# Kernel optimization log

Measured on AMD Instinct MI355X. Metric: run time of the kernel, lower is better.

The kernel has to match this reference:

```python
import jax, jax.numpy as jnp
import numpy as np

NUM_E = 50000
EMBED_DIM = 128
HID_DIM = 200
B = 512
N = 50  # candidate_num / history length
ITER_NUM = 3
ALPHA = 0.5
WEIGHT_BASE = 1.0
SQUASH_W = 1.0
SQUASH_EPS = 1e-9
L2_EPS = 1e-12  # torch F.normalize default eps


def setup_inputs() -> dict:
    key = jax.random.key(0)
    k1, k2, k3, k4, k5, k6, k7 = jax.random.split(key, 7)
    idx = jax.random.randint(k1, (B, N), 0, NUM_E)
    times = jax.random.randint(k2, (B, N), 0, 365)
    # embeddings: normal then row-wise L2 normalize (as in init_embeddings)
    emb = jax.random.normal(k3, (NUM_E, EMBED_DIM), dtype=jnp.float32)
    embeddings = emb / jnp.maximum(jnp.linalg.norm(emb, axis=1, keepdims=True), L2_EPS)
    Ws_w = jax.random.normal(k4, (HID_DIM, EMBED_DIM), dtype=jnp.float32) * (2.0 / (HID_DIM + EMBED_DIM)) ** 0.5
    Ws_b = jnp.zeros((HID_DIM,), dtype=jnp.float32)
    mlp_w = jax.random.normal(k5, (NUM_E, HID_DIM), dtype=jnp.float32) * (2.0 / (NUM_E + HID_DIM)) ** 0.5
    mlp_b = jnp.zeros((NUM_E,), dtype=jnp.float32)
    return {"idx": idx, "times": times, "embeddings": embeddings,
            "Ws_w": Ws_w, "Ws_b": Ws_b, "mlp_w": mlp_w, "mlp_b": mlp_b}


def _squash(s):
    # s: [B, H]; squash over last axis (original axis=-2 on [B,1,1,H,1])
    sq = jnp.sum(s * s, axis=-1, keepdims=True)
    scale = sq / (SQUASH_W + sq) / jnp.sqrt(sq + SQUASH_EPS)
    return scale * s


def reference(idx, times, embeddings, Ws_w, Ws_b, mlp_w, mlp_b):
    # gather history embeddings: [B, N, D]
    embeds = embeddings[idx]
    # temporal weighting -> initial routing logits b_ij: [B, N]
    b = (WEIGHT_BASE + 1.0) / (WEIGHT_BASE + times.astype(jnp.float32))
    # Ws linear (dropout is identity at eval): [B, N, H]
    x = jnp.einsum('bnd,hd->bnh', embeds, Ws_w) + Ws_b
    # u_hat: L2-normalized over H
    u_hat = x / jnp.maximum(jnp.linalg.norm(x, axis=-1, keepdims=True), L2_EPS)
    u_det = jax.lax.stop_gradient(u_hat)
    # dynamic routing, fixed ITER_NUM iterations
    for r in range(ITER_NUM):
        c = jax.nn.softmax(b, axis=1) * N            # [B, N]
        s = jnp.einsum('bn,bnh->bh', c, u_hat)       # [B, H]
        v = _squash(s)                               # [B, H]
        if r < ITER_NUM - 1:
            b = b + jnp.einsum('bnh,bh->bn', u_det, v)
    poses, c_ij = v, c                               # [B, H], [B, N]
    # p_ij: scatter-add c_ij per entity id (math of one_hot^T @ c_ij)
    p = jnp.zeros((B, NUM_E), dtype=jnp.float32)
    p = p.at[jnp.arange(B)[:, None], idx].add(c_ij)
    p = jax.nn.softmax(p, axis=1)
    # decoder mlp (reflect=False)
    scores = poses @ mlp_w.T + mlp_b                 # [B, NUM_E]
    sims = jax.nn.softmax(scores, axis=1)
    return jnp.log(ALPHA * p + (1.0 - ALPHA) * sims)
```

## Files before the change

### kernel.cpp

```cpp
#include <hip/hip_runtime.h>
#include <stdint.h>

#define NUM_E 50000
#define EMBED_DIM 128
#define HID_DIM 200
#define BATCH 512
#define NN 50
#define HPAD 208
#define KPAD 224
#define NKT 7
#define NTT2 3136
#define NXB 196
#define PACK_BLOCKS 784
#define XG_BLOCKS 400

typedef short s16x8 __attribute__((ext_vector_type(8)));
typedef float f32x4 __attribute__((ext_vector_type(4)));

__device__ inline unsigned short f2bf(float f) {
  union { float f; unsigned u; } v; v.f = f;
  unsigned r = v.u + 0x7FFF + ((v.u >> 16) & 1);
  return (unsigned short)(r >> 16);
}
__device__ inline float bf2f(unsigned short b) {
  union { unsigned u; float f; } v; v.u = ((unsigned)b) << 16;
  return v.f;
}

__device__ __forceinline__ void gl_lds16(const unsigned short* g, unsigned short* l) {
  __builtin_amdgcn_global_load_lds(
      (const __attribute__((address_space(1))) unsigned int*)g,
      (__attribute__((address_space(3))) unsigned int*)l, 16, 0, 0);
}

__global__ __launch_bounds__(256) void k_prep(
    const int* __restrict__ idx, const float* __restrict__ emb,
    const float* __restrict__ Ws_w, const float* __restrict__ Ws_b,
    const float* __restrict__ mlp_w,
    unsigned short* __restrict__ Bp, unsigned short* __restrict__ x_ws,
    float* __restrict__ sumsq_ws, float* __restrict__ S_ws)
{
  __shared__ __align__(16) unsigned short smem[12800];
  const int bx = blockIdx.x;
  const int tid = threadIdx.x;

  if (bx < PACK_BLOCKS) {
    const size_t base_f = (size_t)bx * 64 * HID_DIM;
    const float4* src4 = (const float4*)(mlp_w + base_f);
    for (int i = tid; i < 3200; i += 256) {
      float4 f;
      if (base_f + 4 * (size_t)i + 4 <= (size_t)NUM_E * HID_DIM) {
        f = src4[i];
      } else {
        f = make_float4(0.f, 0.f, 0.f, 0.f);
      }
      unsigned short t4[4] __attribute__((aligned(8))) = {
        f2bf(f.x), f2bf(f.y), f2bf(f.z), f2bf(f.w)};
      *(uint2*)&smem[i * 4] = *(uint2*)t4;
    }
    __syncthreads();
    const int nt0 = bx * 4;
    unsigned short* dst = Bp + (size_t)nt0 * NKT * 512;
    for (int s = 0; s < 7; ++s) {
      const int fi = s * 256 + tid;
      const int fr = fi >> 6;
      const int lane = fi & 63;
      const int nt_l = fr / 7, kt = fr - nt_l * 7;
      const int r = nt_l * 16 + (lane & 15);
      const int kb = kt * 32 + (lane >> 4) * 8;
      uint4 val;
      if (kb < HID_DIM) {
        val = *(const uint4*)&smem[r * HID_DIM + kb];
      } else {
        val = make_uint4(0, 0, 0, 0);
      }
      *(uint4*)&dst[(size_t)fi * 8] = val;
    }
    return;
  }
  if (bx >= PACK_BLOCKS + XG_BLOCKS) {
    S_ws[tid] = 0.f;
    S_ws[256 + tid] = 0.f;
    return;
  }

  unsigned short* Al = smem;
  unsigned short* Bl = smem + 64 * 40;
  const int wave = tid >> 6, lane = tid & 63;
  const int q = lane >> 4, l15 = lane & 15;
  const int row0 = (bx - PACK_BLOCKS) * 64;

  f32x4 acc[13];
  for (int i = 0; i < 13; i++) acc[i] = (f32x4){0, 0, 0, 0};

  for (int kt = 0; kt < 4; ++kt) {
    const int k0 = kt * 32;
    {
      const int r = tid >> 2, q4 = tid & 3;
      const int erow = idx[row0 + r];
      const float* src = emb + (size_t)erow * EMBED_DIM + k0 + q4 * 8;
      float4 f0 = *(const float4*)(src);
      float4 f1 = *(const float4*)(src + 4);
      unsigned short tmp[8] __attribute__((aligned(16))) = {
        f2bf(f0.x), f2bf(f0.y), f2bf(f0.z), f2bf(f0.w),
        f2bf(f1.x), f2bf(f1.y), f2bf(f1.z), f2bf(f1.w)};
      *(uint4*)&Al[r * 40 + q4 * 8] = *(uint4*)tmp;
    }
    if (tid < 208) {
      unsigned short tmp[32] __attribute__((aligned(16)));
      if (tid < HID_DIM) {
        const float* src = Ws_w + (size_t)tid * EMBED_DIM + k0;
        for (int j = 0; j < 8; j++) {
          float4 f = *(const float4*)(src + j * 4);
          tmp[j*4+0] = f2bf(f.x); tmp[j*4+1] = f2bf(f.y);
          tmp[j*4+2] = f2bf(f.z); tmp[j*4+3] = f2bf(f.w);
        }
      } else {
        for (int j = 0; j < 32; j++) tmp[j] = 0;
      }
      for (int j = 0; j < 4; j++)
        *(uint4*)&Bl[tid * 40 + j * 8] = *(uint4*)&tmp[j * 8];
    }
    __syncthreads();
    s16x8 a = *(const s16x8*)&Al[(wave * 16 + l15) * 40 + q * 8];
    for (int ni = 0; ni < 13; ++ni) {
      s16x8 bfr = *(const s16x8*)&Bl[(ni * 16 + l15) * 40 + q * 8];
      acc[ni] = __builtin_amdgcn_mfma_f32_16x16x32_bf16(a, bfr, acc[ni], 0, 0, 0);
    }
    __syncthreads();
  }

  float sq[4] = {0, 0, 0, 0};
  for (int ni = 0; ni < 13; ++ni) {
    const int col = ni * 16 + l15;
    const bool cv = col < HID_DIM;
    const float bias = cv ? Ws_b[col] : 0.f;
    for (int p = 0; p < 4; p++) {
      float v = acc[ni][p] + bias;
      if (cv) sq[p] += v * v;
      const int grow = row0 + wave * 16 + q * 4 + p;
      x_ws[(size_t)grow * HPAD + col] = f2bf(cv ? v : 0.f);
    }
  }
  for (int m = 1; m < 16; m <<= 1)
    for (int p = 0; p < 4; p++) sq[p] += __shfl_xor(sq[p], m, 64);
  if (l15 == 0)
    for (int p = 0; p < 4; p++)
      sumsq_ws[row0 + wave * 16 + q * 4 + p] = sq[p];
}

__global__ __launch_bounds__(256) void k_routing(
    const int* __restrict__ idx, const int* __restrict__ times,
    const unsigned short* __restrict__ x_ws, const float* __restrict__ sumsq_ws,
    unsigned short* __restrict__ Ap, float* __restrict__ poses_f,
    float* __restrict__ expa_ws, float* __restrict__ D_ws)
{
  __shared__ float u[NN * 201];
  __shared__ float cc[NN];
  __shared__ float bb[NN];
  __shared__ float vv[HID_DIM];
  __shared__ float nrm[NN];
  __shared__ int   sidx[NN];
  __shared__ float red[4];
  __shared__ float scaleS;
  const int tid = threadIdx.x;
  const int b = blockIdx.x;

  if (tid < NN) {
    nrm[tid] = fmaxf(sqrtf(sumsq_ws[b * NN + tid]), 1e-12f);
    sidx[tid] = idx[b * NN + tid];
    bb[tid] = 2.0f / (1.0f + (float)times[b * NN + tid]);
  }
  __syncthreads();
  const int un = tid >> 2, uc0 = (tid & 3) * 50;
  if (un < NN) {
    const float inv = 1.0f / nrm[un];
    const unsigned short* xs = &x_ws[(size_t)(b * NN + un) * HPAD + uc0];
    for (int j = 0; j < 50; j++) u[un * 201 + uc0 + j] = bf2f(xs[j]) * inv;
  }
  __syncthreads();

  for (int it = 0; it < 3; ++it) {
    if (tid < 64) {
      float x = (tid < NN) ? bb[tid] : -1e30f;
      float m = x;
      for (int d = 1; d < 64; d <<= 1) m = fmaxf(m, __shfl_xor(m, d, 64));
      float e = (tid < NN) ? __expf(x - m) : 0.f;
      float s = e;
      for (int d = 1; d < 64; d <<= 1) s += __shfl_xor(s, d, 64);
      if (tid < NN) cc[tid] = e * (float)NN / s;
    }
    __syncthreads();
    float sh = 0.f;
    if (tid < HID_DIM)
      for (int n = 0; n < NN; n++) sh += cc[n] * u[n * 201 + tid];
    float sq = (tid < HID_DIM) ? sh * sh : 0.f;
    for (int d = 1; d < 64; d <<= 1) sq += __shfl_xor(sq, d, 64);
    if ((tid & 63) == 0) red[tid >> 6] = sq;
    __syncthreads();
    if (tid == 0) {
      const float t = red[0] + red[1] + red[2] + red[3];
      scaleS = t / (1.0f + t) / sqrtf(t + 1e-9f);
    }
    __syncthreads();
    if (tid < HID_DIM) vv[tid] = scaleS * sh;
    __syncthreads();
    if (it < 2) {
      float d = 0.f;
      if (un < NN)
        for (int j = 0; j < 50; j++) d += u[un * 201 + uc0 + j] * vv[uc0 + j];
      d += __shfl_xor(d, 1, 64);
      d += __shfl_xor(d, 2, 64);
      if (un < NN && (tid & 3) == 0) bb[un] += d;
      __syncthreads();
    }
  }
  if (tid < KPAD) {
    const float val = (tid < HID_DIM) ? vv[tid] : 0.f;
    const int kt = tid >> 5, rem = tid & 31, q = rem >> 3, j = rem & 7;
    const int mt = b >> 4, l15 = b & 15;
    Ap[(size_t)(((mt * NKT + kt) * 64) + q * 16 + l15) * 8 + j] = f2bf(val);
  }
  if (tid < HID_DIM) poses_f[b * HID_DIM + tid] = vv[tid];
  if (tid < 64) {
    float a = 0.f; int first = 1;
    const int my = (tid < NN) ? sidx[tid] : -1;
    if (tid < NN) {
      for (int n = 0; n < NN; n++)
        if (sidx[n] == my) { a += cc[n]; if (n < tid) first = 0; }
      expa_ws[b * NN + tid] = __expf(a);
    }
    float contrib = (tid < NN && first) ? (__expf(a) - 1.0f) : 0.f;
    for (int d = 1; d < 64; d <<= 1) contrib += __shfl_xor(contrib, d, 64);
    if (tid == 0) D_ws[b] = (float)NUM_E + contrib;
  }
}

template<int PASS>
__global__ __launch_bounds__(256, 4) void k_gemm(
    const unsigned short* __restrict__ Ap, const unsigned short* __restrict__ Bp,
    const float* __restrict__ mlp_b, const float* __restrict__ D_ws,
    float* __restrict__ S_ws, float* __restrict__ out)
{
  __shared__ __align__(16) unsigned short Bs[16 * 512];
  __shared__ float red[256];
  const int id = blockIdx.x;
  const int yb = id / 200;
  const int xb = id - yb * 200;
  if (xb >= NXB) return;
  const int tid = threadIdx.x;
  const int w = tid >> 6, lane = tid & 63;
  const int q = lane >> 4, l15 = lane & 15;
  const int mt0 = yb * 4;
  const int m0 = yb * 64;
  const int ntb = xb * 16 + w * 4;

  if (PASS == 1 && tid < 64) {
    red[tid]      = 0.5f / D_ws[m0 + tid];
    red[64 + tid] = 0.5f / S_ws[m0 + tid];
  }
  float bias[4];
  #pragma unroll
  for (int nl = 0; nl < 4; ++nl) {
    const int col = (ntb + nl) * 16 + l15;
    bias[nl] = (col < NUM_E) ? mlp_b[col] : 0.f;
  }

  const unsigned short* apBase = Ap + (size_t)mt0 * NKT * 512;

  f32x4 acc[4][4];
  #pragma unroll
  for (int i = 0; i < 4; i++)
    #pragma unroll
    for (int j = 0; j < 4; j++) acc[i][j] = (f32x4){0, 0, 0, 0};

  for (int kt = 0; kt < NKT; ++kt) {
    #pragma unroll
    for (int nl = 0; nl < 4; ++nl)
      gl_lds16(Bp + ((size_t)(ntb + nl) * NKT + kt) * 512 + lane * 8,
               &Bs[(w * 4 + nl) * 512]);
    s16x8 a[4];
    #pragma unroll
    for (int mi = 0; mi < 4; ++mi)
      a[mi] = *(const s16x8*)&apBase[((mi * NKT + kt) * 64 + lane) * 8];
    __syncthreads();
    s16x8 bfr[4];
    #pragma unroll
    for (int nl = 0; nl < 4; ++nl)
      bfr[nl] = *(const s16x8*)&Bs[((w * 4 + nl) * 64 + lane) * 8];
    #pragma unroll
    for (int nl = 0; nl < 4; ++nl)
      #pragma unroll
      for (int mi = 0; mi < 4; ++mi)
        acc[mi][nl] = __builtin_amdgcn_mfma_f32_16x16x32_bf16(a[mi], bfr[nl], acc[mi][nl], 0, 0, 0);
    __syncthreads();
  }

  if (PASS == 0) {
    float rs[4][4];
    #pragma unroll
    for (int mi = 0; mi < 4; mi++)
      #pragma unroll
      for (int p = 0; p < 4; p++) rs[mi][p] = 0.f;
    #pragma unroll
    for (int mi = 0; mi < 4; ++mi)
      #pragma unroll
      for (int nl = 0; nl < 4; ++nl) {
        const int col = (ntb + nl) * 16 + l15;
        #pragma unroll
        for (int p = 0; p < 4; p++) {
          const float v = acc[mi][nl][p] + bias[nl];
          rs[mi][p] += (col < NUM_E) ? __expf(v) : 0.f;
        }
      }
    #pragma unroll
    for (int m = 1; m < 16; m <<= 1)
      for (int mi = 0; mi < 4; mi++)
        for (int p = 0; p < 4; p++)
          rs[mi][p] += __shfl_xor(rs[mi][p], m, 64);
    if (l15 == 0)
      for (int mi = 0; mi < 4; mi++)
        for (int p = 0; p < 4; p++)
          red[w * 64 + mi * 16 + q * 4 + p] = rs[mi][p];
    __syncthreads();
    if (tid < 64)
      atomicAdd(&S_ws[m0 + tid],
                red[tid] + red[64 + tid] + red[128 + tid] + red[192 + tid]);
  } else {
    #pragma unroll
    for (int mi = 0; mi < 4; ++mi) {
      #pragma unroll
      for (int p = 0; p < 4; p++) {
        const int rl = mi * 16 + q * 4 + p;
        const float invD = red[rl];
        const float invS = red[64 + rl];
        const int row = m0 + rl;
        #pragma unroll
        for (int nl = 0; nl < 4; ++nl) {
          const int col = (ntb + nl) * 16 + l15;
          if (col < NUM_E) {
            const float v = acc[mi][nl][p] + bias[nl];
            out[(size_t)row * NUM_E + col] = __logf(fmaf(__expf(v), invS, invD));
          }
        }
      }
    }
  }
}

__global__ __launch_bounds__(256) void k_fix(
    const int* __restrict__ idx, const float* __restrict__ expa,
    const float* __restrict__ poses_f, const float* __restrict__ mlp_w,
    const float* __restrict__ mlp_b, const float* __restrict__ D_ws,
    const float* __restrict__ S_ws, float* __restrict__ out)
{
  const int t = blockIdx.x * 4 + (threadIdx.x >> 6);
  const int lane = threadIdx.x & 63;
  if (t >= BATCH * NN) return;
  const int b = t / NN;
  const int j = idx[t];
  float dot = 0.f;
  for (int h = lane; h < HID_DIM; h += 64)
    dot += poses_f[b * HID_DIM + h] * mlp_w[(size_t)j * HID_DIM + h];
  for (int m = 1; m < 64; m <<= 1) dot += __shfl_xor(dot, m, 64);
  if (lane == 0) {
    const float s = dot + mlp_b[j];
    out[(size_t)b * NUM_E + j] = __logf(0.5f * expa[t] / D_ws[b] +
                                        0.5f * __expf(s) / S_ws[b]);
  }
}

extern "C" void kernel_launch(void* const* d_in, const int* in_sizes, int n_in,
                              void* d_out, int out_size, void* d_ws, size_t ws_size,
                              hipStream_t stream) {
  const int*   idx   = (const int*)d_in[0];
  const int*   times = (const int*)d_in[1];
  const float* emb   = (const float*)d_in[2];
  const float* Ws_w  = (const float*)d_in[3];
  const float* Ws_b  = (const float*)d_in[4];
  const float* mlp_w = (const float*)d_in[5];
  const float* mlp_b = (const float*)d_in[6];
  float* out = (float*)d_out;

  char* ws = (char*)d_ws;
  unsigned short* Bp    = (unsigned short*)ws; ws += (size_t)NTT2 * NKT * 64 * 8 * 2;
  unsigned short* x_ws  = (unsigned short*)ws; ws += (size_t)BATCH * NN * HPAD * 2;
  unsigned short* Ap    = (unsigned short*)ws; ws += (size_t)32 * NKT * 64 * 8 * 2;
  float* poses_f        = (float*)ws;          ws += (size_t)BATCH * HID_DIM * 4;
  float* sumsq          = (float*)ws;          ws += (size_t)BATCH * NN * 4;
  float* expa           = (float*)ws;          ws += (size_t)BATCH * NN * 4;
  float* D_ws           = (float*)ws;          ws += (size_t)BATCH * 4;
  float* S_ws           = (float*)ws;          ws += (size_t)BATCH * 4;

  k_prep   <<<dim3(PACK_BLOCKS + XG_BLOCKS + 1), 256, 0, stream>>>(
      idx, emb, Ws_w, Ws_b, mlp_w, Bp, x_ws, sumsq, S_ws);
  k_routing<<<dim3(BATCH),        256, 0, stream>>>(idx, times, x_ws, sumsq, Ap, poses_f, expa, D_ws);
  k_gemm<0><<<dim3(1600),         256, 0, stream>>>(Ap, Bp, mlp_b, D_ws, S_ws, out);
  k_gemm<1><<<dim3(1600),         256, 0, stream>>>(Ap, Bp, mlp_b, D_ws, S_ws, out);
  k_fix    <<<dim3(BATCH * NN / 4), 256, 0, stream>>>(idx, expa, poses_f, mlp_w, mlp_b, D_ws, S_ws, out);
}
```

Measured before the change: 266.4 us.

## Fuse all stages into one persistent cooperative kernel with grid syncs

Replaces the five-kernel pipeline with a single cooperative persistent kernel. It loops over work units (per-batch routing with the Ws projection done inline, mlp_w packing, S init), then runs the two GEMM passes and the fix-up pass, with grid.sync between phases. Each batch now computes its own 50 embedding projections directly, and the x_ws round trip is removed. The aim is to cut launch overhead and intermediate global traffic. In exchange the grid is capped at 768 blocks with occupancy 3, so GEMM tiles loop persistently and LDS use is larger. It falls back to the old kernels if the cooperative launch fails.

```diff
diff --git a/kernel.cpp b/kernel.cpp
--- a/kernel.cpp
+++ b/kernel.cpp
@@ -1,5 +1,8 @@
 #include <hip/hip_runtime.h>
+#include <hip/hip_cooperative_groups.h>
 #include <stdint.h>
+
+namespace cg = cooperative_groups;
 
 #define NUM_E 50000
 #define EMBED_DIM 128
@@ -11,8 +14,12 @@
 #define NKT 7
 #define NTT2 3136
 #define NXB 196
-#define PACK_BLOCKS 784
-#define XG_BLOCKS 400
+#define NTILES 1600
+#define PACK_UNITS 784
+#define BATCH_UNITS 512
+#define NUNITS (BATCH_UNITS + PACK_UNITS + 1)
+#define USTRIDE 201
+#define MAXGRID 768
 
 typedef short s16x8 __attribute__((ext_vector_type(8)));
 typedef float f32x4 __attribute__((ext_vector_type(4)));
@@ -32,6 +39,348 @@
       (const __attribute__((address_space(1))) unsigned int*)g,
       (__attribute__((address_space(3))) unsigned int*)l, 16, 0, 0);
 }
+
+template<int PASS>
+__device__ __forceinline__ void gemm_tile(
+    int yb, int xb, char* buf, int tid,
+    const unsigned short* Ap, const unsigned short* Bp, const float* mlp_b,
+    const float* D_ws, float* S_ws, float* out)
+{
+  unsigned short* Bs = (unsigned short*)buf;
+  float* red = (float*)(buf + 16384);
+  const int w = tid >> 6, lane = tid & 63;
+  const int q = lane >> 4, l15 = lane & 15;
+  const int mt0 = yb * 4;
+  const int m0 = yb * 64;
+  const int ntb = xb * 16 + w * 4;
+
+  __syncthreads();
+  if (PASS == 1 && tid < 64) {
+    red[tid]      = 0.5f / D_ws[m0 + tid];
+    red[64 + tid] = 0.5f / S_ws[m0 + tid];
+  }
+  float bias[4];
+  #pragma unroll
+  for (int nl = 0; nl < 4; ++nl) {
+    const int col = (ntb + nl) * 16 + l15;
+    bias[nl] = (col < NUM_E) ? mlp_b[col] : 0.f;
+  }
+  const unsigned short* apBase = Ap + (size_t)mt0 * NKT * 512;
+
+  f32x4 acc[4][4];
+  #pragma unroll
+  for (int i = 0; i < 4; i++)
+    #pragma unroll
+    for (int j = 0; j < 4; j++) acc[i][j] = (f32x4){0, 0, 0, 0};
+
+  for (int kt = 0; kt < NKT; ++kt) {
+    #pragma unroll
+    for (int nl = 0; nl < 4; ++nl)
+      gl_lds16(Bp + ((size_t)(ntb + nl) * NKT + kt) * 512 + lane * 8,
+               &Bs[(w * 4 + nl) * 512]);
+    s16x8 a[4];
+    #pragma unroll
+    for (int mi = 0; mi < 4; ++mi)
+      a[mi] = *(const s16x8*)&apBase[((mi * NKT + kt) * 64 + lane) * 8];
+    __syncthreads();
+    s16x8 bfr[4];
+    #pragma unroll
+    for (int nl = 0; nl < 4; ++nl)
+      bfr[nl] = *(const s16x8*)&Bs[((w * 4 + nl) * 64 + lane) * 8];
+    #pragma unroll
+    for (int nl = 0; nl < 4; ++nl)
+      #pragma unroll
+      for (int mi = 0; mi < 4; ++mi)
+        acc[mi][nl] = __builtin_amdgcn_mfma_f32_16x16x32_bf16(a[mi], bfr[nl], acc[mi][nl], 0, 0, 0);
+    __syncthreads();
+  }
+
+  if (PASS == 0) {
+    float rs[4][4];
+    #pragma unroll
+    for (int mi = 0; mi < 4; mi++)
+      #pragma unroll
+      for (int p = 0; p < 4; p++) rs[mi][p] = 0.f;
+    #pragma unroll
+    for (int mi = 0; mi < 4; ++mi)
+      #pragma unroll
+      for (int nl = 0; nl < 4; ++nl) {
+        const int col = (ntb + nl) * 16 + l15;
+        #pragma unroll
+        for (int p = 0; p < 4; p++) {
+          const float v = acc[mi][nl][p] + bias[nl];
+          rs[mi][p] += (col < NUM_E) ? __expf(v) : 0.f;
+        }
+      }
+    #pragma unroll
+    for (int m = 1; m < 16; m <<= 1)
+      for (int mi = 0; mi < 4; mi++)
+        for (int p = 0; p < 4; p++)
+          rs[mi][p] += __shfl_xor(rs[mi][p], m, 64);
+    if (l15 == 0)
+      for (int mi = 0; mi < 4; mi++)
+        for (int p = 0; p < 4; p++)
+          red[w * 64 + mi * 16 + q * 4 + p] = rs[mi][p];
+    __syncthreads();
+    if (tid < 64)
+      atomicAdd(&S_ws[m0 + tid],
+                red[tid] + red[64 + tid] + red[128 + tid] + red[192 + tid]);
+  } else {
+    #pragma unroll
+    for (int mi = 0; mi < 4; ++mi) {
+      #pragma unroll
+      for (int p = 0; p < 4; p++) {
+        const int rl = mi * 16 + q * 4 + p;
+        const float invD = red[rl];
+        const float invS = red[64 + rl];
+        const int row = m0 + rl;
+        #pragma unroll
+        for (int nl = 0; nl < 4; ++nl) {
+          const int col = (ntb + nl) * 16 + l15;
+          if (col < NUM_E) {
+            const float v = acc[mi][nl][p] + bias[nl];
+            out[(size_t)row * NUM_E + col] = __logf(fmaf(__expf(v), invS, invD));
+          }
+        }
+      }
+    }
+  }
+}
+
+__global__ __launch_bounds__(256, 3) void k_all(
+    const int* __restrict__ idx, const int* __restrict__ times,
+    const float* __restrict__ emb, const float* __restrict__ Ws_w,
+    const float* __restrict__ Ws_b, const float* __restrict__ mlp_w,
+    const float* __restrict__ mlp_b, float* __restrict__ out,
+    unsigned short* __restrict__ Bp, unsigned short* __restrict__ Ap,
+    float* __restrict__ poses_f, float* __restrict__ expa_ws,
+    float* __restrict__ D_ws, float* __restrict__ S_ws)
+{
+  __shared__ __align__(16) char buf[40320];
+  __shared__ float cc[NN], bb[NN], vv[HID_DIM], red4[4], scaleS;
+  __shared__ int sidx[NN];
+  const int tid = threadIdx.x;
+  const int w = tid >> 6, lane = tid & 63;
+  const int q = lane >> 4, l15 = lane & 15;
+  cg::grid_group grid = cg::this_grid();
+
+  for (int u = blockIdx.x; u < NUNITS; u += gridDim.x) {
+    __syncthreads();
+    if (u < BATCH_UNITS) {
+      const int b = u;
+      if (tid < NN) {
+        sidx[tid] = idx[b * NN + tid];
+        bb[tid] = 2.0f / (1.0f + (float)times[b * NN + tid]);
+      }
+      __syncthreads();
+      unsigned short* Afr = (unsigned short*)buf;
+      unsigned short* Bfr = (unsigned short*)(buf + 16384);
+      for (int v = tid; v < 1024; v += 256) {
+        const int row = v >> 4, c = v & 15;
+        const int kt = c >> 2, qq = c & 3;
+        unsigned short tmp[8] __attribute__((aligned(16)));
+        if (row < NN) {
+          const float* src = emb + (size_t)sidx[row] * EMBED_DIM + c * 8;
+          float4 f0 = *(const float4*)src;
+          float4 f1 = *(const float4*)(src + 4);
+          tmp[0] = f2bf(f0.x); tmp[1] = f2bf(f0.y); tmp[2] = f2bf(f0.z); tmp[3] = f2bf(f0.w);
+          tmp[4] = f2bf(f1.x); tmp[5] = f2bf(f1.y); tmp[6] = f2bf(f1.z); tmp[7] = f2bf(f1.w);
+        } else {
+          for (int j = 0; j < 8; j++) tmp[j] = 0;
+        }
+        *(uint4*)&Afr[(((row >> 4) * 4 + kt) * 64 + qq * 16 + (row & 15)) * 8] = *(uint4*)tmp;
+      }
+      f32x4 acc[4][4];
+      #pragma unroll
+      for (int i = 0; i < 4; i++)
+        #pragma unroll
+        for (int j = 0; j < 4; j++) acc[i][j] = (f32x4){0, 0, 0, 0};
+      __syncthreads();
+      for (int kt = 0; kt < 4; ++kt) {
+        for (int v = tid; v < 832; v += 256) {
+          const int n = v >> 2, cq = v & 3;
+          unsigned short tmp[8] __attribute__((aligned(16)));
+          if (n < HID_DIM) {
+            const float* src = Ws_w + (size_t)n * EMBED_DIM + kt * 32 + cq * 8;
+            float4 f0 = *(const float4*)src;
+            float4 f1 = *(const float4*)(src + 4);
+            tmp[0] = f2bf(f0.x); tmp[1] = f2bf(f0.y); tmp[2] = f2bf(f0.z); tmp[3] = f2bf(f0.w);
+            tmp[4] = f2bf(f1.x); tmp[5] = f2bf(f1.y); tmp[6] = f2bf(f1.z); tmp[7] = f2bf(f1.w);
+          } else {
+            for (int j = 0; j < 8; j++) tmp[j] = 0;
+          }
+          *(uint4*)&Bfr[((n >> 4) * 64 + cq * 16 + (n & 15)) * 8] = *(uint4*)tmp;
+        }
+        __syncthreads();
+        s16x8 a[4];
+        #pragma unroll
+        for (int mt = 0; mt < 4; ++mt)
+          a[mt] = *(const s16x8*)&Afr[((mt * 4 + kt) * 64 + lane) * 8];
+        #pragma unroll
+        for (int ii = 0; ii < 4; ++ii) {
+          const int nt = w + ii * 4;
+          if (nt < 13) {
+            s16x8 bv = *(const s16x8*)&Bfr[(nt * 64 + lane) * 8];
+            #pragma unroll
+            for (int mt = 0; mt < 4; ++mt)
+              acc[mt][ii] = __builtin_amdgcn_mfma_f32_16x16x32_bf16(a[mt], bv, acc[mt][ii], 0, 0, 0);
+          }
+        }
+        __syncthreads();
+      }
+      float* uu = (float*)buf;
+      #pragma unroll
+      for (int ii = 0; ii < 4; ++ii) {
+        const int nt = w + ii * 4;
+        if (nt < 13) {
+          const int col = nt * 16 + l15;
+          if (col < HID_DIM) {
+            const float bv = Ws_b[col];
+            #pragma unroll
+            for (int mt = 0; mt < 4; ++mt)
+              #pragma unroll
+              for (int p = 0; p < 4; p++) {
+                const int row = mt * 16 + q * 4 + p;
+                if (row < NN) uu[row * USTRIDE + col] = acc[mt][ii][p] + bv;
+              }
+          }
+        }
+      }
+      __syncthreads();
+      const int un = tid >> 2, uc0 = (tid & 3) * 50;
+      if (un < NN) {
+        float s = 0.f;
+        for (int j = 0; j < 50; j++) {
+          const float x = uu[un * USTRIDE + uc0 + j];
+          s += x * x;
+        }
+        s += __shfl_xor(s, 1, 64);
+        s += __shfl_xor(s, 2, 64);
+        const float inv = 1.0f / fmaxf(sqrtf(s), 1e-12f);
+        for (int j = 0; j < 50; j++) uu[un * USTRIDE + uc0 + j] *= inv;
+      }
+      __syncthreads();
+      for (int it = 0; it < 3; ++it) {
+        if (tid < 64) {
+          float x = (tid < NN) ? bb[tid] : -1e30f;
+          float m = x;
+          for (int d = 1; d < 64; d <<= 1) m = fmaxf(m, __shfl_xor(m, d, 64));
+          float e = (tid < NN) ? __expf(x - m) : 0.f;
+          float s = e;
+          for (int d = 1; d < 64; d <<= 1) s += __shfl_xor(s, d, 64);
+          if (tid < NN) cc[tid] = e * (float)NN / s;
+        }
+        __syncthreads();
+        float sh = 0.f;
+        if (tid < HID_DIM)
+          for (int n = 0; n < NN; n++) sh += cc[n] * uu[n * USTRIDE + tid];
+        float sq2 = (tid < HID_DIM) ? sh * sh : 0.f;
+        for (int d = 1; d < 64; d <<= 1) sq2 += __shfl_xor(sq2, d, 64);
+        if ((tid & 63) == 0) red4[tid >> 6] = sq2;
+        __syncthreads();
+        if (tid == 0) {
+          const float t2 = red4[0] + red4[1] + red4[2] + red4[3];
+          scaleS = t2 / (1.0f + t2) / sqrtf(t2 + 1e-9f);
+        }
+        __syncthreads();
+        if (tid < HID_DIM) vv[tid] = scaleS * sh;
+        __syncthreads();
+        if (it < 2) {
+          float d = 0.f;
+          if (un < NN)
+            for (int j = 0; j < 50; j++)
+              d += uu[un * USTRIDE + uc0 + j] * vv[uc0 + j];
+          d += __shfl_xor(d, 1, 64);
+          d += __shfl_xor(d, 2, 64);
+          if (un < NN && (tid & 3) == 0) bb[un] += d;
+          __syncthreads();
+        }
+      }
+      if (tid < KPAD) {
+        const float val = (tid < HID_DIM) ? vv[tid] : 0.f;
+        const int kt = tid >> 5, rem = tid & 31, qq = rem >> 3, j = rem & 7;
+        const int mt = b >> 4, ll = b & 15;
+        Ap[(size_t)(((mt * NKT + kt) * 64) + qq * 16 + ll) * 8 + j] = f2bf(val);
+      }
+      if (tid < HID_DIM) poses_f[b * HID_DIM + tid] = vv[tid];
+      if (tid < 64) {
+        float a2 = 0.f; int first = 1;
+        const int my = (tid < NN) ? sidx[tid] : -1;
+        if (tid < NN) {
+          for (int n = 0; n < NN; n++)
+            if (sidx[n] == my) { a2 += cc[n]; if (n < tid) first = 0; }
+          expa_ws[b * NN + tid] = __expf(a2);
+        }
+        float contrib = (tid < NN && first) ? (__expf(a2) - 1.0f) : 0.f;
+        for (int d = 1; d < 64; d <<= 1) contrib += __shfl_xor(contrib, d, 64);
+        if (tid == 0) D_ws[b] = (float)NUM_E + contrib;
+      }
+    } else if (u < BATCH_UNITS + PACK_UNITS) {
+      const int pb = u - BATCH_UNITS;
+      unsigned short* smem = (unsigned short*)buf;
+      const size_t base_f = (size_t)pb * 64 * HID_DIM;
+      const float4* src4 = (const float4*)(mlp_w + base_f);
+      for (int i = tid; i < 3200; i += 256) {
+        float4 f;
+        if (base_f + 4 * (size_t)i + 4 <= (size_t)NUM_E * HID_DIM) f = src4[i];
+        else f = make_float4(0.f, 0.f, 0.f, 0.f);
+        unsigned short t4[4] __attribute__((aligned(8))) = {
+          f2bf(f.x), f2bf(f.y), f2bf(f.z), f2bf(f.w)};
+        *(uint2*)&smem[i * 4] = *(uint2*)t4;
+      }
+      __syncthreads();
+      const int nt0 = pb * 4;
+      unsigned short* dst = Bp + (size_t)nt0 * NKT * 512;
+      for (int s2 = 0; s2 < 7; ++s2) {
+        const int fi = s2 * 256 + tid;
+        const int fr = fi >> 6;
+        const int ln = fi & 63;
+        const int nt_l = fr / 7, kt = fr - nt_l * 7;
+        const int r = nt_l * 16 + (ln & 15);
+        const int kb = kt * 32 + (ln >> 4) * 8;
+        uint4 val;
+        if (kb < HID_DIM) val = *(const uint4*)&smem[r * HID_DIM + kb];
+        else val = make_uint4(0, 0, 0, 0);
+        *(uint4*)&dst[(size_t)fi * 8] = val;
+      }
+    } else {
+      S_ws[tid] = 0.f;
+      S_ws[256 + tid] = 0.f;
+    }
+  }
+  grid.sync();
+
+  for (int t = blockIdx.x; t < NTILES; t += gridDim.x) {
+    const int yb = t / 200, xb = t - yb * 200;
+    if (xb < NXB)
+      gemm_tile<0>(yb, xb, buf, tid, Ap, Bp, mlp_b, D_ws, S_ws, out);
+  }
+  grid.sync();
+
+  for (int t = blockIdx.x; t < NTILES; t += gridDim.x) {
+    const int yb = t / 200, xb = t - yb * 200;
+    if (xb < NXB)
+      gemm_tile<1>(yb, xb, buf, tid, Ap, Bp, mlp_b, D_ws, S_ws, out);
+  }
+  grid.sync();
+
+  for (int s = blockIdx.x * 4 + w; s < BATCH * NN; s += gridDim.x * 4) {
+    const int b = s / NN;
+    const int j = idx[s];
+    float dot = 0.f;
+    for (int h = lane; h < HID_DIM; h += 64)
+      dot += poses_f[b * HID_DIM + h] * mlp_w[(size_t)j * HID_DIM + h];
+    for (int m = 1; m < 64; m <<= 1) dot += __shfl_xor(dot, m, 64);
+    if (lane == 0) {
+      const float sc = dot + mlp_b[j];
+      out[(size_t)b * NUM_E + j] = __logf(0.5f * expa_ws[s] / D_ws[b] +
+                                          0.5f * __expf(sc) / S_ws[b]);
+    }
+  }
+}
+
+#define PACK_BLOCKS 784
+#define XG_BLOCKS 400
 
 __global__ __launch_bounds__(256) void k_prep(
     const int* __restrict__ idx, const float* __restrict__ emb,
@@ -49,11 +398,8 @@
     const float4* src4 = (const float4*)(mlp_w + base_f);
     for (int i = tid; i < 3200; i += 256) {
       float4 f;
-      if (base_f + 4 * (size_t)i + 4 <= (size_t)NUM_E * HID_DIM) {
-        f = src4[i];
-      } else {
-        f = make_float4(0.f, 0.f, 0.f, 0.f);
-      }
+      if (base_f + 4 * (size_t)i + 4 <= (size_t)NUM_E * HID_DIM) f = src4[i];
+      else f = make_float4(0.f, 0.f, 0.f, 0.f);
       unsigned short t4[4] __attribute__((aligned(8))) = {
         f2bf(f.x), f2bf(f.y), f2bf(f.z), f2bf(f.w)};
       *(uint2*)&smem[i * 4] = *(uint2*)t4;
@@ -64,16 +410,13 @@
     for (int s = 0; s < 7; ++s) {
       const int fi = s * 256 + tid;
       const int fr = fi >> 6;
-      const int lane = fi & 63;
+      const int ln = fi & 63;
       const int nt_l = fr / 7, kt = fr - nt_l * 7;
-      const int r = nt_l * 16 + (lane & 15);
-      const int kb = kt * 32 + (lane >> 4) * 8;
+      const int r = nt_l * 16 + (ln & 15);
+      const int kb = kt * 32 + (ln >> 4) * 8;
       uint4 val;
-      if (kb < HID_DIM) {
-        val = *(const uint4*)&smem[r * HID_DIM + kb];
-      } else {
-        val = make_uint4(0, 0, 0, 0);
-      }
+      if (kb < HID_DIM) val = *(const uint4*)&smem[r * HID_DIM + kb];
+      else val = make_uint4(0, 0, 0, 0);
       *(uint4*)&dst[(size_t)fi * 8] = val;
     }
     return;
@@ -83,7 +426,6 @@
     S_ws[256 + tid] = 0.f;
     return;
   }
-
   unsigned short* Al = smem;
   unsigned short* Bl = smem + 64 * 40;
   const int wave = tid >> 6, lane = tid & 63;
@@ -242,110 +584,12 @@
     const float* __restrict__ mlp_b, const float* __restrict__ D_ws,
     float* __restrict__ S_ws, float* __restrict__ out)
 {
-  __shared__ __align__(16) unsigned short Bs[16 * 512];
-  __shared__ float red[256];
+  __shared__ __align__(16) char buf2[17920];
   const int id = blockIdx.x;
   const int yb = id / 200;
   const int xb = id - yb * 200;
   if (xb >= NXB) return;
-  const int tid = threadIdx.x;
-  const int w = tid >> 6, lane = tid & 63;
-  const int q = lane >> 4, l15 = lane & 15;
-  const int mt0 = yb * 4;
-  const int m0 = yb * 64;
-  const int ntb = xb * 16 + w * 4;
-
-  if (PASS == 1 && tid < 64) {
-    red[tid]      = 0.5f / D_ws[m0 + tid];
-    red[64 + tid] = 0.5f / S_ws[m0 + tid];
-  }
-  float bias[4];
-  #pragma unroll
-  for (int nl = 0; nl < 4; ++nl) {
-    const int col = (ntb + nl) * 16 + l15;
-    bias[nl] = (col < NUM_E) ? mlp_b[col] : 0.f;
-  }
-
-  const unsigned short* apBase = Ap + (size_t)mt0 * NKT * 512;
-
-  f32x4 acc[4][4];
-  #pragma unroll
-  for (int i = 0; i < 4; i++)
-    #pragma unroll
-    for (int j = 0; j < 4; j++) acc[i][j] = (f32x4){0, 0, 0, 0};
-
-  for (int kt = 0; kt < NKT; ++kt) {
-    #pragma unroll
-    for (int nl = 0; nl < 4; ++nl)
-      gl_lds16(Bp + ((size_t)(ntb + nl) * NKT + kt) * 512 + lane * 8,
-               &Bs[(w * 4 + nl) * 512]);
-    s16x8 a[4];
-    #pragma unroll
-    for (int mi = 0; mi < 4; ++mi)
-      a[mi] = *(const s16x8*)&apBase[((mi * NKT + kt) * 64 + lane) * 8];
-    __syncthreads();
-    s16x8 bfr[4];
-    #pragma unroll
-    for (int nl = 0; nl < 4; ++nl)
-      bfr[nl] = *(const s16x8*)&Bs[((w * 4 + nl) * 64 + lane) * 8];
-    #pragma unroll
-    for (int nl = 0; nl < 4; ++nl)
-      #pragma unroll
-      for (int mi = 0; mi < 4; ++mi)
-        acc[mi][nl] = __builtin_amdgcn_mfma_f32_16x16x32_bf16(a[mi], bfr[nl], acc[mi][nl], 0, 0, 0);
-    __syncthreads();
-  }
-
-  if (PASS == 0) {
-    float rs[4][4];
-    #pragma unroll
-    for (int mi = 0; mi < 4; mi++)
-      #pragma unroll
-      for (int p = 0; p < 4; p++) rs[mi][p] = 0.f;
-    #pragma unroll
-    for (int mi = 0; mi < 4; ++mi)
-      #pragma unroll
-      for (int nl = 0; nl < 4; ++nl) {
-        const int col = (ntb + nl) * 16 + l15;
-        #pragma unroll
-        for (int p = 0; p < 4; p++) {
-          const float v = acc[mi][nl][p] + bias[nl];
-          rs[mi][p] += (col < NUM_E) ? __expf(v) : 0.f;
-        }
-      }
-    #pragma unroll
-    for (int m = 1; m < 16; m <<= 1)
-      for (int mi = 0; mi < 4; mi++)
-        for (int p = 0; p < 4; p++)
-          rs[mi][p] += __shfl_xor(rs[mi][p], m, 64);
-    if (l15 == 0)
-      for (int mi = 0; mi < 4; mi++)
-        for (int p = 0; p < 4; p++)
-          red[w * 64 + mi * 16 + q * 4 + p] = rs[mi][p];
-    __syncthreads();
-    if (tid < 64)
-      atomicAdd(&S_ws[m0 + tid],
-                red[tid] + red[64 + tid] + red[128 + tid] + red[192 + tid]);
-  } else {
-    #pragma unroll
-    for (int mi = 0; mi < 4; ++mi) {
-      #pragma unroll
-      for (int p = 0; p < 4; p++) {
-        const int rl = mi * 16 + q * 4 + p;
-        const float invD = red[rl];
-        const float invS = red[64 + rl];
-        const int row = m0 + rl;
-        #pragma unroll
-        for (int nl = 0; nl < 4; ++nl) {
-          const int col = (ntb + nl) * 16 + l15;
-          if (col < NUM_E) {
-            const float v = acc[mi][nl][p] + bias[nl];
-            out[(size_t)row * NUM_E + col] = __logf(fmaf(__expf(v), invS, invD));
-          }
-        }
-      }
-    }
-  }
+  gemm_tile<PASS>(yb, xb, buf2, threadIdx.x, Ap, Bp, mlp_b, D_ws, S_ws, out);
 }
 
 __global__ __launch_bounds__(256) void k_fix(
@@ -392,6 +636,19 @@
   float* D_ws           = (float*)ws;          ws += (size_t)BATCH * 4;
   float* S_ws           = (float*)ws;          ws += (size_t)BATCH * 4;
 
+  int nb = 0;
+  hipError_t qerr = hipOccupancyMaxActiveBlocksPerMultiprocessor(&nb, k_all, 256, 0);
+  if (qerr != hipSuccess || nb < 1) nb = 1;
+  int g = nb * 256;
+  if (g > MAXGRID) g = MAXGRID;
+
+  void* args[] = {
+    (void*)&idx, (void*)&times, (void*)&emb, (void*)&Ws_w, (void*)&Ws_b,
+    (void*)&mlp_w, (void*)&mlp_b, (void*)&out, (void*)&Bp, (void*)&Ap,
+    (void*)&poses_f, (void*)&expa, (void*)&D_ws, (void*)&S_ws};
+  hipError_t err = hipLaunchCooperativeKernel(k_all, dim3(g), dim3(256), args, 0, stream);
+  if (err == hipSuccess) return;
+
   k_prep   <<<dim3(PACK_BLOCKS + XG_BLOCKS + 1), 256, 0, stream>>>(
       idx, emb, Ws_w, Ws_b, mlp_w, Bp, x_ws, sumsq, S_ws);
   k_routing<<<dim3(BATCH),        256, 0, stream>>>(idx, times, x_ws, sumsq, Ap, poses_f, expa, D_ws);
```

Result: slower. 474.3 us (+78.1%).

## Fuse Ws projection into per-batch routing kernel and drop the x workspace

Applied to the files above, without the earlier changes.

Merges the embedding-gather Ws GEMM and the dynamic-routing step into one per-batch block, keeping u in LDS instead of writing bf16 x and sumsq to global and reading them back. The mlp_w packing blocks are launched in the same grid, which removes one kernel launch. Each routing block now recomputes the 50x200 projection with MFMA and computes the norms locally. This needs about 40KB of LDS per block, which may lower occupancy, and u is now kept in fp32 after the bf16 MFMA instead of being rounded back to bf16.

```diff
diff --git a/kernel.cpp b/kernel.cpp
--- a/kernel.cpp
+++ b/kernel.cpp
@@ -6,13 +6,12 @@
 #define HID_DIM 200
 #define BATCH 512
 #define NN 50
-#define HPAD 208
 #define KPAD 224
 #define NKT 7
 #define NTT2 3136
 #define NXB 196
-#define PACK_BLOCKS 784
-#define XG_BLOCKS 400
+#define PACK_UNITS 784
+#define USTRIDE 201
 
 typedef short s16x8 __attribute__((ext_vector_type(8)));
 typedef float f32x4 __attribute__((ext_vector_type(4)));
@@ -33,222 +32,14 @@
       (__attribute__((address_space(3))) unsigned int*)l, 16, 0, 0);
 }
 
-__global__ __launch_bounds__(256) void k_prep(
-    const int* __restrict__ idx, const float* __restrict__ emb,
-    const float* __restrict__ Ws_w, const float* __restrict__ Ws_b,
-    const float* __restrict__ mlp_w,
-    unsigned short* __restrict__ Bp, unsigned short* __restrict__ x_ws,
-    float* __restrict__ sumsq_ws, float* __restrict__ S_ws)
+template<int PASS>
+__device__ __forceinline__ void gemm_tile(
+    int yb, int xb, char* buf, int tid,
+    const unsigned short* Ap, const unsigned short* Bp, const float* mlp_b,
+    const float* D_ws, float* S_ws, float* out)
 {
-  __shared__ __align__(16) unsigned short smem[12800];
-  const int bx = blockIdx.x;
-  const int tid = threadIdx.x;
-
-  if (bx < PACK_BLOCKS) {
-    const size_t base_f = (size_t)bx * 64 * HID_DIM;
-    const float4* src4 = (const float4*)(mlp_w + base_f);
-    for (int i = tid; i < 3200; i += 256) {
-      float4 f;
-      if (base_f + 4 * (size_t)i + 4 <= (size_t)NUM_E * HID_DIM) {
-        f = src4[i];
-      } else {
-        f = make_float4(0.f, 0.f, 0.f, 0.f);
-      }
-      unsigned short t4[4] __attribute__((aligned(8))) = {
-        f2bf(f.x), f2bf(f.y), f2bf(f.z), f2bf(f.w)};
-      *(uint2*)&smem[i * 4] = *(uint2*)t4;
-    }
-    __syncthreads();
-    const int nt0 = bx * 4;
-    unsigned short* dst = Bp + (size_t)nt0 * NKT * 512;
-    for (int s = 0; s < 7; ++s) {
-      const int fi = s * 256 + tid;
-      const int fr = fi >> 6;
-      const int lane = fi & 63;
-      const int nt_l = fr / 7, kt = fr - nt_l * 7;
-      const int r = nt_l * 16 + (lane & 15);
-      const int kb = kt * 32 + (lane >> 4) * 8;
-      uint4 val;
-      if (kb < HID_DIM) {
-        val = *(const uint4*)&smem[r * HID_DIM + kb];
-      } else {
-        val = make_uint4(0, 0, 0, 0);
-      }
-      *(uint4*)&dst[(size_t)fi * 8] = val;
-    }
-    return;
-  }
-  if (bx >= PACK_BLOCKS + XG_BLOCKS) {
-    S_ws[tid] = 0.f;
-    S_ws[256 + tid] = 0.f;
-    return;
-  }
-
-  unsigned short* Al = smem;
-  unsigned short* Bl = smem + 64 * 40;
-  const int wave = tid >> 6, lane = tid & 63;
-  const int q = lane >> 4, l15 = lane & 15;
-  const int row0 = (bx - PACK_BLOCKS) * 64;
-
-  f32x4 acc[13];
-  for (int i = 0; i < 13; i++) acc[i] = (f32x4){0, 0, 0, 0};
-
-  for (int kt = 0; kt < 4; ++kt) {
-    const int k0 = kt * 32;
-    {
-      const int r = tid >> 2, q4 = tid & 3;
-      const int erow = idx[row0 + r];
-      const float* src = emb + (size_t)erow * EMBED_DIM + k0 + q4 * 8;
-      float4 f0 = *(const float4*)(src);
-      float4 f1 = *(const float4*)(src + 4);
-      unsigned short tmp[8] __attribute__((aligned(16))) = {
-        f2bf(f0.x), f2bf(f0.y), f2bf(f0.z), f2bf(f0.w),
-        f2bf(f1.x), f2bf(f1.y), f2bf(f1.z), f2bf(f1.w)};
-      *(uint4*)&Al[r * 40 + q4 * 8] = *(uint4*)tmp;
-    }
-    if (tid < 208) {
-      unsigned short tmp[32] __attribute__((aligned(16)));
-      if (tid < HID_DIM) {
-        const float* src = Ws_w + (size_t)tid * EMBED_DIM + k0;
-        for (int j = 0; j < 8; j++) {
-          float4 f = *(const float4*)(src + j * 4);
-          tmp[j*4+0] = f2bf(f.x); tmp[j*4+1] = f2bf(f.y);
-          tmp[j*4+2] = f2bf(f.z); tmp[j*4+3] = f2bf(f.w);
-        }
-      } else {
-        for (int j = 0; j < 32; j++) tmp[j] = 0;
-      }
-      for (int j = 0; j < 4; j++)
-        *(uint4*)&Bl[tid * 40 + j * 8] = *(uint4*)&tmp[j * 8];
-    }
-    __syncthreads();
-    s16x8 a = *(const s16x8*)&Al[(wave * 16 + l15) * 40 + q * 8];
-    for (int ni = 0; ni < 13; ++ni) {
-      s16x8 bfr = *(const s16x8*)&Bl[(ni * 16 + l15) * 40 + q * 8];
-      acc[ni] = __builtin_amdgcn_mfma_f32_16x16x32_bf16(a, bfr, acc[ni], 0, 0, 0);
-    }
-    __syncthreads();
-  }
-
-  float sq[4] = {0, 0, 0, 0};
-  for (int ni = 0; ni < 13; ++ni) {
-    const int col = ni * 16 + l15;
-    const bool cv = col < HID_DIM;
-    const float bias = cv ? Ws_b[col] : 0.f;
-    for (int p = 0; p < 4; p++) {
-      float v = acc[ni][p] + bias;
-      if (cv) sq[p] += v * v;
-      const int grow = row0 + wave * 16 + q * 4 + p;
-      x_ws[(size_t)grow * HPAD + col] = f2bf(cv ? v : 0.f);
-    }
-  }
-  for (int m = 1; m < 16; m <<= 1)
-    for (int p = 0; p < 4; p++) sq[p] += __shfl_xor(sq[p], m, 64);
-  if (l15 == 0)
-    for (int p = 0; p < 4; p++)
-      sumsq_ws[row0 + wave * 16 + q * 4 + p] = sq[p];
-}
-
-__global__ __launch_bounds__(256) void k_routing(
-    const int* __restrict__ idx, const int* __restrict__ times,
-    const unsigned short* __restrict__ x_ws, const float* __restrict__ sumsq_ws,
-    unsigned short* __restrict__ Ap, float* __restrict__ poses_f,
-    float* __restrict__ expa_ws, float* __restrict__ D_ws)
-{
-  __shared__ float u[NN * 201];
-  __shared__ float cc[NN];
-  __shared__ float bb[NN];
-  __shared__ float vv[HID_DIM];
-  __shared__ float nrm[NN];
-  __shared__ int   sidx[NN];
-  __shared__ float red[4];
-  __shared__ float scaleS;
-  const int tid = threadIdx.x;
-  const int b = blockIdx.x;
-
-  if (tid < NN) {
-    nrm[tid] = fmaxf(sqrtf(sumsq_ws[b * NN + tid]), 1e-12f);
-    sidx[tid] = idx[b * NN + tid];
-    bb[tid] = 2.0f / (1.0f + (float)times[b * NN + tid]);
-  }
-  __syncthreads();
-  const int un = tid >> 2, uc0 = (tid & 3) * 50;
-  if (un < NN) {
-    const float inv = 1.0f / nrm[un];
-    const unsigned short* xs = &x_ws[(size_t)(b * NN + un) * HPAD + uc0];
-    for (int j = 0; j < 50; j++) u[un * 201 + uc0 + j] = bf2f(xs[j]) * inv;
-  }
-  __syncthreads();
-
-  for (int it = 0; it < 3; ++it) {
-    if (tid < 64) {
-      float x = (tid < NN) ? bb[tid] : -1e30f;
-      float m = x;
-      for (int d = 1; d < 64; d <<= 1) m = fmaxf(m, __shfl_xor(m, d, 64));
-      float e = (tid < NN) ? __expf(x - m) : 0.f;
-      float s = e;
-      for (int d = 1; d < 64; d <<= 1) s += __shfl_xor(s, d, 64);
-      if (tid < NN) cc[tid] = e * (float)NN / s;
-    }
-    __syncthreads();
-    float sh = 0.f;
-    if (tid < HID_DIM)
-      for (int n = 0; n < NN; n++) sh += cc[n] * u[n * 201 + tid];
-    float sq = (tid < HID_DIM) ? sh * sh : 0.f;
-    for (int d = 1; d < 64; d <<= 1) sq += __shfl_xor(sq, d, 64);
-    if ((tid & 63) == 0) red[tid >> 6] = sq;
-    __syncthreads();
-    if (tid == 0) {
-      const float t = red[0] + red[1] + red[2] + red[3];
-      scaleS = t / (1.0f + t) / sqrtf(t + 1e-9f);
-    }
-    __syncthreads();
-    if (tid < HID_DIM) vv[tid] = scaleS * sh;
-    __syncthreads();
-    if (it < 2) {
-      float d = 0.f;
-      if (un < NN)
-        for (int j = 0; j < 50; j++) d += u[un * 201 + uc0 + j] * vv[uc0 + j];
-      d += __shfl_xor(d, 1, 64);
-      d += __shfl_xor(d, 2, 64);
-      if (un < NN && (tid & 3) == 0) bb[un] += d;
-      __syncthreads();
-    }
-  }
-  if (tid < KPAD) {
-    const float val = (tid < HID_DIM) ? vv[tid] : 0.f;
-    const int kt = tid >> 5, rem = tid & 31, q = rem >> 3, j = rem & 7;
-    const int mt = b >> 4, l15 = b & 15;
-    Ap[(size_t)(((mt * NKT + kt) * 64) + q * 16 + l15) * 8 + j] = f2bf(val);
-  }
-  if (tid < HID_DIM) poses_f[b * HID_DIM + tid] = vv[tid];
-  if (tid < 64) {
-    float a = 0.f; int first = 1;
-    const int my = (tid < NN) ? sidx[tid] : -1;
-    if (tid < NN) {
-      for (int n = 0; n < NN; n++)
-        if (sidx[n] == my) { a += cc[n]; if (n < tid) first = 0; }
-      expa_ws[b * NN + tid] = __expf(a);
-    }
-    float contrib = (tid < NN && first) ? (__expf(a) - 1.0f) : 0.f;
-    for (int d = 1; d < 64; d <<= 1) contrib += __shfl_xor(contrib, d, 64);
-    if (tid == 0) D_ws[b] = (float)NUM_E + contrib;
-  }
-}
-
-template<int PASS>
-__global__ __launch_bounds__(256, 4) void k_gemm(
-    const unsigned short* __restrict__ Ap, const unsigned short* __restrict__ Bp,
-    const float* __restrict__ mlp_b, const float* __restrict__ D_ws,
-    float* __restrict__ S_ws, float* __restrict__ out)
-{
-  __shared__ __align__(16) unsigned short Bs[16 * 512];
-  __shared__ float red[256];
-  const int id = blockIdx.x;
-  const int yb = id / 200;
-  const int xb = id - yb * 200;
-  if (xb >= NXB) return;
-  const int tid = threadIdx.x;
+  unsigned short* Bs = (unsigned short*)buf;
+  float* red = (float*)(buf + 16384);
   const int w = tid >> 6, lane = tid & 63;
   const int q = lane >> 4, l15 = lane & 15;
   const int mt0 = yb * 4;
@@ -265,7 +56,6 @@
     const int col = (ntb + nl) * 16 + l15;
     bias[nl] = (col < NUM_E) ? mlp_b[col] : 0.f;
   }
-
   const unsigned short* apBase = Ap + (size_t)mt0 * NKT * 512;
 
   f32x4 acc[4][4];
@@ -346,6 +136,219 @@
       }
     }
   }
+}
+
+__global__ __launch_bounds__(256, 3) void k_stage1(
+    const int* __restrict__ idx, const int* __restrict__ times,
+    const float* __restrict__ emb, const float* __restrict__ Ws_w,
+    const float* __restrict__ Ws_b, const float* __restrict__ mlp_w,
+    unsigned short* __restrict__ Bp, unsigned short* __restrict__ Ap,
+    float* __restrict__ poses_f, float* __restrict__ expa_ws,
+    float* __restrict__ D_ws, float* __restrict__ S_ws)
+{
+  __shared__ __align__(16) char buf[40320];
+  __shared__ float cc[NN], bb[NN], vv[HID_DIM], red4[4], scaleS;
+  __shared__ int sidx[NN];
+  const int u = blockIdx.x;
+  const int tid = threadIdx.x;
+  const int w = tid >> 6, lane = tid & 63;
+  const int q = lane >> 4, l15 = lane & 15;
+
+  if (u < BATCH) {
+    const int b = u;
+    if (tid < NN) {
+      sidx[tid] = idx[b * NN + tid];
+      bb[tid] = 2.0f / (1.0f + (float)times[b * NN + tid]);
+    }
+    __syncthreads();
+    unsigned short* Afr = (unsigned short*)buf;
+    unsigned short* Bfr = (unsigned short*)(buf + 16384);
+    for (int v = tid; v < 1024; v += 256) {
+      const int row = v >> 4, c = v & 15;
+      const int kt = c >> 2, qq = c & 3;
+      unsigned short tmp[8] __attribute__((aligned(16)));
+      if (row < NN) {
+        const float* src = emb + (size_t)sidx[row] * EMBED_DIM + c * 8;
+        float4 f0 = *(const float4*)src;
+        float4 f1 = *(const float4*)(src + 4);
+        tmp[0] = f2bf(f0.x); tmp[1] = f2bf(f0.y); tmp[2] = f2bf(f0.z); tmp[3] = f2bf(f0.w);
+        tmp[4] = f2bf(f1.x); tmp[5] = f2bf(f1.y); tmp[6] = f2bf(f1.z); tmp[7] = f2bf(f1.w);
+      } else {
+        for (int j = 0; j < 8; j++) tmp[j] = 0;
+      }
+      *(uint4*)&Afr[(((row >> 4) * 4 + kt) * 64 + qq * 16 + (row & 15)) * 8] = *(uint4*)tmp;
+    }
+    f32x4 acc[4][4];
+    #pragma unroll
+    for (int i = 0; i < 4; i++)
+      #pragma unroll
+      for (int j = 0; j < 4; j++) acc[i][j] = (f32x4){0, 0, 0, 0};
+    __syncthreads();
+    for (int kt = 0; kt < 4; ++kt) {
+      for (int v = tid; v < 832; v += 256) {
+        const int n = v >> 2, cq = v & 3;
+        unsigned short tmp[8] __attribute__((aligned(16)));
+        if (n < HID_DIM) {
+          const float* src = Ws_w + (size_t)n * EMBED_DIM + kt * 32 + cq * 8;
+          float4 f0 = *(const float4*)src;
+          float4 f1 = *(const float4*)(src + 4);
+          tmp[0] = f2bf(f0.x); tmp[1] = f2bf(f0.y); tmp[2] = f2bf(f0.z); tmp[3] = f2bf(f0.w);
+          tmp[4] = f2bf(f1.x); tmp[5] = f2bf(f1.y); tmp[6] = f2bf(f1.z); tmp[7] = f2bf(f1.w);
+        } else {
+          for (int j = 0; j < 8; j++) tmp[j] = 0;
+        }
+        *(uint4*)&Bfr[((n >> 4) * 64 + cq * 16 + (n & 15)) * 8] = *(uint4*)tmp;
+      }
+      __syncthreads();
+      s16x8 a[4];
+      #pragma unroll
+      for (int mt = 0; mt < 4; ++mt)
+        a[mt] = *(const s16x8*)&Afr[((mt * 4 + kt) * 64 + lane) * 8];
+      #pragma unroll
+      for (int ii = 0; ii < 4; ++ii) {
+        const int nt = w + ii * 4;
+        if (nt < 13) {
+          s16x8 bv = *(const s16x8*)&Bfr[(nt * 64 + lane) * 8];
+          #pragma unroll
+          for (int mt = 0; mt < 4; ++mt)
+            acc[mt][ii] = __builtin_amdgcn_mfma_f32_16x16x32_bf16(a[mt], bv, acc[mt][ii], 0, 0, 0);
+        }
+      }
+      __syncthreads();
+    }
+    float* uu = (float*)buf;
+    #pragma unroll
+    for (int ii = 0; ii < 4; ++ii) {
+      const int nt = w + ii * 4;
+      if (nt < 13) {
+        const int col = nt * 16 + l15;
+        if (col < HID_DIM) {
+          const float bv = Ws_b[col];
+          #pragma unroll
+          for (int mt = 0; mt < 4; ++mt)
+            #pragma unroll
+            for (int p = 0; p < 4; p++) {
+              const int row = mt * 16 + q * 4 + p;
+              if (row < NN) uu[row * USTRIDE + col] = acc[mt][ii][p] + bv;
+            }
+        }
+      }
+    }
+    __syncthreads();
+    const int un = tid >> 2, uc0 = (tid & 3) * 50;
+    if (un < NN) {
+      float s = 0.f;
+      for (int j = 0; j < 50; j++) {
+        const float x = uu[un * USTRIDE + uc0 + j];
+        s += x * x;
+      }
+      s += __shfl_xor(s, 1, 64);
+      s += __shfl_xor(s, 2, 64);
+      const float inv = 1.0f / fmaxf(sqrtf(s), 1e-12f);
+      for (int j = 0; j < 50; j++) uu[un * USTRIDE + uc0 + j] *= inv;
+    }
+    __syncthreads();
+    for (int it = 0; it < 3; ++it) {
+      if (tid < 64) {
+        float x = (tid < NN) ? bb[tid] : -1e30f;
+        float m = x;
+        for (int d = 1; d < 64; d <<= 1) m = fmaxf(m, __shfl_xor(m, d, 64));
+        float e = (tid < NN) ? __expf(x - m) : 0.f;
+        float s = e;
+        for (int d = 1; d < 64; d <<= 1) s += __shfl_xor(s, d, 64);
+        if (tid < NN) cc[tid] = e * (float)NN / s;
+      }
+      __syncthreads();
+      float sh = 0.f;
+      if (tid < HID_DIM)
+        for (int n = 0; n < NN; n++) sh += cc[n] * uu[n * USTRIDE + tid];
+      float sq2 = (tid < HID_DIM) ? sh * sh : 0.f;
+      for (int d = 1; d < 64; d <<= 1) sq2 += __shfl_xor(sq2, d, 64);
+      if ((tid & 63) == 0) red4[tid >> 6] = sq2;
+      __syncthreads();
+      if (tid == 0) {
+        const float t2 = red4[0] + red4[1] + red4[2] + red4[3];
+        scaleS = t2 / (1.0f + t2) / sqrtf(t2 + 1e-9f);
+      }
+      __syncthreads();
+      if (tid < HID_DIM) vv[tid] = scaleS * sh;
+      __syncthreads();
+      if (it < 2) {
+        float d = 0.f;
+        if (un < NN)
+          for (int j = 0; j < 50; j++)
+            d += uu[un * USTRIDE + uc0 + j] * vv[uc0 + j];
+        d += __shfl_xor(d, 1, 64);
+        d += __shfl_xor(d, 2, 64);
+        if (un < NN && (tid & 3) == 0) bb[un] += d;
+        __syncthreads();
+      }
+    }
+    if (tid < KPAD) {
+      const float val = (tid < HID_DIM) ? vv[tid] : 0.f;
+      const int kt = tid >> 5, rem = tid & 31, qq = rem >> 3, j = rem & 7;
+      const int mt = b >> 4, ll = b & 15;
+      Ap[(size_t)(((mt * NKT + kt) * 64) + qq * 16 + ll) * 8 + j] = f2bf(val);
+    }
+    if (tid < HID_DIM) poses_f[b * HID_DIM + tid] = vv[tid];
+    if (tid < 64) {
+      float a2 = 0.f; int first = 1;
+      const int my = (tid < NN) ? sidx[tid] : -1;
+      if (tid < NN) {
+        for (int n = 0; n < NN; n++)
+          if (sidx[n] == my) { a2 += cc[n]; if (n < tid) first = 0; }
+        expa_ws[b * NN + tid] = __expf(a2);
+      }
+      float contrib = (tid < NN && first) ? (__expf(a2) - 1.0f) : 0.f;
+      for (int d = 1; d < 64; d <<= 1) contrib += __shfl_xor(contrib, d, 64);
+      if (tid == 0) D_ws[b] = (float)NUM_E + contrib;
+    }
+  } else if (u < BATCH + PACK_UNITS) {
+    const int pb = u - BATCH;
+    unsigned short* smem = (unsigned short*)buf;
+    const size_t base_f = (size_t)pb * 64 * HID_DIM;
+    const float4* src4 = (const float4*)(mlp_w + base_f);
+    for (int i = tid; i < 3200; i += 256) {
+      float4 f;
+      if (base_f + 4 * (size_t)i + 4 <= (size_t)NUM_E * HID_DIM) f = src4[i];
+      else f = make_float4(0.f, 0.f, 0.f, 0.f);
+      unsigned short t4[4] __attribute__((aligned(8))) = {
+        f2bf(f.x), f2bf(f.y), f2bf(f.z), f2bf(f.w)};
+      *(uint2*)&smem[i * 4] = *(uint2*)t4;
+    }
+    __syncthreads();
+    const int nt0 = pb * 4;
+    unsigned short* dst = Bp + (size_t)nt0 * NKT * 512;
+    for (int s2 = 0; s2 < 7; ++s2) {
+      const int fi = s2 * 256 + tid;
+      const int fr = fi >> 6;
+      const int ln = fi & 63;
+      const int nt_l = fr / 7, kt = fr - nt_l * 7;
+      const int r = nt_l * 16 + (ln & 15);
+      const int kb = kt * 32 + (ln >> 4) * 8;
+      uint4 val;
+      if (kb < HID_DIM) val = *(const uint4*)&smem[r * HID_DIM + kb];
+      else val = make_uint4(0, 0, 0, 0);
+      *(uint4*)&dst[(size_t)fi * 8] = val;
+    }
+  } else {
+    S_ws[tid] = 0.f;
+    S_ws[256 + tid] = 0.f;
+  }
+}
+
+template<int PASS>
+__global__ __launch_bounds__(256, 4) void k_gemm(
+    const unsigned short* __restrict__ Ap, const unsigned short* __restrict__ Bp,
+    const float* __restrict__ mlp_b, const float* __restrict__ D_ws,
+    float* __restrict__ S_ws, float* __restrict__ out)
+{
+  __shared__ __align__(16) char buf2[17408];
+  const int id = blockIdx.x;
+  const int yb = id / 200;
+  const int xb = id - yb * 200;
+  if (xb >= NXB) return;
+  gemm_tile<PASS>(yb, xb, buf2, threadIdx.x, Ap, Bp, mlp_b, D_ws, S_ws, out);
 }
 
 __global__ __launch_bounds__(256) void k_fix(
@@ -384,18 +387,15 @@
 
   char* ws = (char*)d_ws;
   unsigned short* Bp    = (unsigned short*)ws; ws += (size_t)NTT2 * NKT * 64 * 8 * 2;
-  unsigned short* x_ws  = (unsigned short*)ws; ws += (size_t)BATCH * NN * HPAD * 2;
   unsigned short* Ap    = (unsigned short*)ws; ws += (size_t)32 * NKT * 64 * 8 * 2;
   float* poses_f        = (float*)ws;          ws += (size_t)BATCH * HID_DIM * 4;
-  float* sumsq          = (float*)ws;          ws += (size_t)BATCH * NN * 4;
   float* expa           = (float*)ws;          ws += (size_t)BATCH * NN * 4;
   float* D_ws           = (float*)ws;          ws += (size_t)BATCH * 4;
   float* S_ws           = (float*)ws;          ws += (size_t)BATCH * 4;
 
-  k_prep   <<<dim3(PACK_BLOCKS + XG_BLOCKS + 1), 256, 0, stream>>>(
-      idx, emb, Ws_w, Ws_b, mlp_w, Bp, x_ws, sumsq, S_ws);
-  k_routing<<<dim3(BATCH),        256, 0, stream>>>(idx, times, x_ws, sumsq, Ap, poses_f, expa, D_ws);
-  k_gemm<0><<<dim3(1600),         256, 0, stream>>>(Ap, Bp, mlp_b, D_ws, S_ws, out);
-  k_gemm<1><<<dim3(1600),         256, 0, stream>>>(Ap, Bp, mlp_b, D_ws, S_ws, out);
+  k_stage1 <<<dim3(BATCH + PACK_UNITS + 1), 256, 0, stream>>>(
+      idx, times, emb, Ws_w, Ws_b, mlp_w, Bp, Ap, poses_f, expa, D_ws, S_ws);
+  k_gemm<0><<<dim3(1600),           256, 0, stream>>>(Ap, Bp, mlp_b, D_ws, S_ws, out);
+  k_gemm<1><<<dim3(1600),           256, 0, stream>>>(Ap, Bp, mlp_b, D_ws, S_ws, out);
   k_fix    <<<dim3(BATCH * NN / 4), 256, 0, stream>>>(idx, expa, poses_f, mlp_w, mlp_b, D_ws, S_ws, out);
 }
```

Result: faster. 256.4 us (-3.7%).
